# Kernel optimization log

Hardware: AMD Instinct MI355X
Metric: run time of the kernel (lower is better)

The kernel has to match this reference:

```python
import jax, jax.numpy as jnp
import numpy as np

B, S, D = 16, 1024, 128
V = 100000
N = 4096


def _l2norm(x, eps=1e-12):
    # matches torch F.normalize(dim=-1): x / max(||x||, eps)
    n = jnp.sqrt(jnp.sum(x * x, axis=-1, keepdims=True))
    return x / jnp.maximum(n, eps)


def setup_inputs() -> dict:
    key = jax.random.key(0)
    k1, k2, k3, k4, k5 = jax.random.split(key, 5)
    query_embeddings = jax.random.normal(k1, (B, S, D), dtype=jnp.float32)
    key_embeddings = jax.random.normal(k2, (V, D), dtype=jnp.float32)
    loc_b = jax.random.randint(k3, (N,), 0, B)
    loc_s = jax.random.randint(k4, (N,), 0, S)
    label_locations = jnp.stack([loc_b, loc_s], axis=1).astype(jnp.int64)
    labels = jax.random.randint(k5, (N,), 0, V).astype(jnp.int64)
    return {
        "query_embeddings": query_embeddings,
        "key_embeddings": key_embeddings,
        "label_locations": label_locations,
        "labels": labels,
    }


def reference(query_embeddings, key_embeddings, label_locations, labels):
    # gather query vectors at label positions -> [N, D]
    q = query_embeddings[label_locations[:, 0], label_locations[:, 1]]
    q = _l2norm(q)
    k = _l2norm(key_embeddings)
    logits = jnp.einsum("nd,vd->nv", q, k)  # [N, V]
    logZ = jax.nn.logsumexp(logits, axis=-1)  # [N]
    true_logit = jnp.take_along_axis(logits, labels[:, None], axis=-1)[:, 0]
    loss = jnp.mean(logZ - true_logit)  # CrossEntropyLoss mean reduction
    return loss
```

## Files before the change

kernel.cpp:

```cpp
#include <hip/hip_runtime.h>
#include <hip/hip_bf16.h>
#include <hip/hip_fp8.h>

#define S_ 1024
#define D_ 128
#define V_ 100000
#define VSTRIPS_ 3136
#define NPHASE_ 32
#define N_ 4096
#define PADROWS_ 352.0f

typedef __attribute__((ext_vector_type(4))) float f32x4;
typedef __attribute__((ext_vector_type(4))) int   i32x4;
typedef __attribute__((ext_vector_type(8))) int   i32x8;

#define LOG2E_ 1.4426950408889634f
#define LN2_   0.6931471805599453f

__device__ __forceinline__ float exp2_fast(float x) {
#if __has_builtin(__builtin_amdgcn_exp2f)
    return __builtin_amdgcn_exp2f(x);
#else
    return exp2f(x);
#endif
}

__device__ __forceinline__ unsigned char to_fp8(float x) {
    __hip_fp8_e4m3 t(x);
    return (unsigned char)t.__x;
}
__device__ __forceinline__ float from_fp8(unsigned char b) {
    __hip_fp8_e4m3 t; t.__x = (__hip_fp8_storage_t)b;
    return (float)t;
}

__global__ void knorm_kernel(const float* __restrict__ K, char* __restrict__ Kn) {
    __shared__ char sm[4096];
    const int strip = blockIdx.x;
    const int tid = threadIdx.x;
    const int lane = tid & 63;
    const int wvv = tid >> 6;
    char* dst = Kn + (size_t)strip * 4096;
    if (strip >= 3125) {
        *(f32x4*)(dst + tid * 16) = (f32x4){0.f, 0.f, 0.f, 0.f};
        return;
    }
    #pragma unroll
    for (int i = 0; i < 8; ++i) {
        int r = wvv * 8 + i;
        float2 v = ((const float2*)(K + ((size_t)strip * 32 + r) * D_))[lane];
        float ss = v.x * v.x + v.y * v.y;
        #pragma unroll
        for (int off = 32; off; off >>= 1) ss += __shfl_xor(ss, off);
        float rn = rsqrtf(ss);
        unsigned short pk = (unsigned short)to_fp8(v.x * rn)
                          | ((unsigned short)to_fp8(v.y * rn) << 8);
        int addr = ((r >> 4) << 11) + (((lane >> 3) & 1) << 10)
                 + (((lane >> 4) * 16 + (r & 15)) << 4) + ((lane & 7) << 1);
        *(unsigned short*)(sm + addr) = pk;
    }
    __syncthreads();
    *(f32x4*)(dst + tid * 16) = *(const f32x4*)(sm + tid * 16);
}

__global__ void qnorm_kernel(const float* __restrict__ Q, const int* __restrict__ loc,
                             char* __restrict__ Qn, float* __restrict__ Ssum) {
    int w = (blockIdx.x * blockDim.x + threadIdx.x) >> 6;
    int lane = threadIdx.x & 63;
    if (w >= N_) return;
    if (lane == 0) Ssum[w] = 0.f;
    int b = loc[2 * w], s = loc[2 * w + 1];
    float2 v = ((const float2*)(Q + ((size_t)b * S_ + (size_t)s) * D_))[lane];
    float ss = v.x * v.x + v.y * v.y;
    #pragma unroll
    for (int off = 32; off; off >>= 1) ss += __shfl_xor(ss, off);
    float rn = rsqrtf(ss) * LOG2E_;
    unsigned short pk = (unsigned short)to_fp8(v.x * rn)
                      | ((unsigned short)to_fp8(v.y * rn) << 8);
    *(unsigned short*)(Qn + (size_t)w * 128 + 2 * lane) = pk;
}

__global__ __launch_bounds__(256, 2) void ce_main(
    const char* __restrict__ Qn,
    const char* __restrict__ Kn,
    float* __restrict__ Ssum)
{
    const int tid  = threadIdx.x;
    const int lane = tid & 63;
    const int wv   = tid >> 6;
    const int r0   = lane & 15;
    const int hi   = lane >> 4;

    const int fid   = blockIdx.y * 32 + blockIdx.x;
    const int xcd   = fid & 7;
    const int idx   = fid >> 3;
    const int phase = xcd * 4 + (idx >> 5);
    const int qb    = idx & 31;

    i32x8 afr[2];
    {
        const char* qsrc = Qn + ((size_t)qb * 128 + wv * 32 + r0) * 128 + (hi << 5);
        #pragma unroll
        for (int m = 0; m < 2; ++m) {
            i32x4 lo = *(const i32x4*)(qsrc + m * 2048);
            i32x4 hh = *(const i32x4*)(qsrc + m * 2048 + 16);
            afr[m] = (i32x8){lo[0], lo[1], lo[2], lo[3], hh[0], hh[1], hh[2], hh[3]};
        }
    }

    const char* kvbase = Kn + (size_t)phase * 4096 + (lane << 4);

#define LOADSET(B0, B1, j) do {                                              \
        const char* p = kvbase + (size_t)(j) * (4096 * NPHASE_);             \
        i32x4 t0 = *(const i32x4*)(p);                                       \
        i32x4 t1 = *(const i32x4*)(p + 1024);                                \
        i32x4 t2 = *(const i32x4*)(p + 2048);                                \
        i32x4 t3 = *(const i32x4*)(p + 3072);                                \
        B0 = (i32x8){t0[0], t0[1], t0[2], t0[3], t1[0], t1[1], t1[2], t1[3]};\
        B1 = (i32x8){t2[0], t2[1], t2[2], t2[3], t3[0], t3[1], t3[2], t3[3]};\
    } while (0)

#define COMPUTE(B0, B1, ACC) do {                                            \
        __builtin_amdgcn_s_setprio(1);                                       \
        ACC[0][0] = __builtin_amdgcn_mfma_scale_f32_16x16x128_f8f6f4(        \
            afr[0], B0, fz, 0, 0, 0, 127, 0, 127);                           \
        ACC[0][1] = __builtin_amdgcn_mfma_scale_f32_16x16x128_f8f6f4(        \
            afr[0], B1, fz, 0, 0, 0, 127, 0, 127);                           \
        ACC[1][0] = __builtin_amdgcn_mfma_scale_f32_16x16x128_f8f6f4(        \
            afr[1], B0, fz, 0, 0, 0, 127, 0, 127);                           \
        ACC[1][1] = __builtin_amdgcn_mfma_scale_f32_16x16x128_f8f6f4(        \
            afr[1], B1, fz, 0, 0, 0, 127, 0, 127);                           \
        __builtin_amdgcn_s_setprio(0);                                       \
    } while (0)

#define EXP2S(ACC) do {                                                      \
        _Pragma("unroll")                                                    \
        for (int m = 0; m < 2; ++m)                                          \
            _Pragma("unroll")                                                \
            for (int q = 0; q < 4; ++q)                                      \
                psum[m][q] += exp2_fast(ACC[m][0][q]) + exp2_fast(ACC[m][1][q]); \
    } while (0)

    float psum[2][4];
    #pragma unroll
    for (int m = 0; m < 2; ++m)
        #pragma unroll
        for (int q = 0; q < 4; ++q) psum[m][q] = 0.f;

    const f32x4 fz = {0.f, 0.f, 0.f, 0.f};
    f32x4 accE[2][2], accO[2][2];
    #pragma unroll
    for (int m = 0; m < 2; ++m)
        #pragma unroll
        for (int nn = 0; nn < 2; ++nn)
            accO[m][nn] = (f32x4){-16384.f, -16384.f, -16384.f, -16384.f};

    i32x8 RA0, RA1, RB0, RB1;
    LOADSET(RA0, RA1, 0);
    #pragma unroll 1
    for (int j = 0; j < 96; j += 2) {
        LOADSET(RB0, RB1, j + 1);
        EXP2S(accO);
        COMPUTE(RA0, RA1, accE);
        LOADSET(RA0, RA1, j + 2);
        EXP2S(accE);
        COMPUTE(RB0, RB1, accO);
    }
    LOADSET(RB0, RB1, 97);
    EXP2S(accO);
    COMPUTE(RA0, RA1, accE);
    EXP2S(accE);
    COMPUTE(RB0, RB1, accO);
    EXP2S(accO);

#undef LOADSET
#undef COMPUTE
#undef EXP2S

    #pragma unroll
    for (int m = 0; m < 2; ++m) {
        #pragma unroll
        for (int q = 0; q < 4; ++q) {
            float v = psum[m][q];
            v += __shfl_xor(v, 1);
            v += __shfl_xor(v, 2);
            v += __shfl_xor(v, 4);
            v += __shfl_xor(v, 8);
            if (r0 == 0) {
                int row = qb * 128 + wv * 32 + m * 16 + hi * 4 + q;
                atomicAdd(&Ssum[row], v);
            }
        }
    }
}

__global__ void term_kernel(const char* __restrict__ Qn,
                            const char* __restrict__ Kn,
                            const int* __restrict__ labels,
                            const float* __restrict__ Ssum,
                            float* __restrict__ T) {
    int w = (blockIdx.x * blockDim.x + threadIdx.x) >> 6;
    int lane = threadIdx.x & 63;
    if (w >= N_) return;
    int lab = labels[w];
    const unsigned char* qp = (const unsigned char*)(Qn + (size_t)w * 128 + 2 * lane);
    const unsigned char* kp = (const unsigned char*)(Kn
                      + ((size_t)(lab >> 5)) * 4096 + (((lab >> 4) & 1) << 11)
                      + (((lane >> 3) & 1) << 10)
                      + (((lane >> 4) * 16 + (lab & 15)) << 4) + ((lane & 7) << 1));
    float d = from_fp8(qp[0]) * from_fp8(kp[0])
            + from_fp8(qp[1]) * from_fp8(kp[1]);
    #pragma unroll
    for (int off = 32; off; off >>= 1) d += __shfl_xor(d, off);
    if (lane == 0) T[w] = logf(Ssum[w] - PADROWS_) - d * LN2_;
}

__global__ void reduce_kernel(const float* __restrict__ T, float* __restrict__ out) {
    __shared__ float sm[4];
    float s = 0.f;
    for (int i = threadIdx.x; i < N_; i += 256) s += T[i];
    #pragma unroll
    for (int off = 32; off; off >>= 1) s += __shfl_xor(s, off);
    if ((threadIdx.x & 63) == 0) sm[threadIdx.x >> 6] = s;
    __syncthreads();
    if (threadIdx.x == 0) out[0] = (sm[0] + sm[1] + sm[2] + sm[3]) * (1.0f / (float)N_);
}

extern "C" void kernel_launch(void* const* d_in, const int* in_sizes, int n_in,
                              void* d_out, int out_size, void* d_ws, size_t ws_size,
                              hipStream_t stream) {
    (void)in_sizes; (void)n_in; (void)out_size; (void)ws_size;
    const float* Q   = (const float*)d_in[0];
    const float* K   = (const float*)d_in[1];
    const int* loc   = (const int*)d_in[2];
    const int* labels= (const int*)d_in[3];
    float* out = (float*)d_out;

    char* ws = (char*)d_ws;
    char* Kn    = ws;
    char* Qn    = ws + 12845056;
    float* Ssum = (float*)(ws + 12845056 + 524288);
    float* T    = Ssum + N_;

    knorm_kernel<<<VSTRIPS_, 256, 0, stream>>>(K, Kn);
    qnorm_kernel<<<N_ / 4, 256, 0, stream>>>(Q, loc, Qn, Ssum);
    ce_main<<<dim3(32, NPHASE_), 256, 0, stream>>>(Qn, Kn, Ssum);
    term_kernel<<<N_ / 4, 256, 0, stream>>>(Qn, Kn, labels, Ssum, T);
    reduce_kernel<<<1, 256, 0, stream>>>(T, out);
}
```

Baseline: 86.50 us.

## Merge K/Q normalization into one prep kernel and use 32-byte contiguous fp8 tiles

```diff
diff --git a/kernel.cpp b/kernel.cpp
--- a/kernel.cpp
+++ b/kernel.cpp
@@ -34,50 +34,50 @@
     return (float)t;
 }
 
-__global__ void knorm_kernel(const float* __restrict__ K, char* __restrict__ Kn) {
+__global__ void prep_kernel(const float* __restrict__ K, const float* __restrict__ Q,
+                            const int* __restrict__ loc,
+                            char* __restrict__ Kn, char* __restrict__ Qn,
+                            float* __restrict__ Ssum) {
     __shared__ char sm[4096];
-    const int strip = blockIdx.x;
+    const int bid = blockIdx.x;
     const int tid = threadIdx.x;
     const int lane = tid & 63;
     const int wvv = tid >> 6;
-    char* dst = Kn + (size_t)strip * 4096;
-    if (strip >= 3125) {
-        *(f32x4*)(dst + tid * 16) = (f32x4){0.f, 0.f, 0.f, 0.f};
-        return;
-    }
-    #pragma unroll
-    for (int i = 0; i < 8; ++i) {
-        int r = wvv * 8 + i;
-        float2 v = ((const float2*)(K + ((size_t)strip * 32 + r) * D_))[lane];
+    if (bid < VSTRIPS_) {
+        char* dst = Kn + (size_t)bid * 4096;
+        if (bid >= 3125) {
+            *(f32x4*)(dst + tid * 16) = (f32x4){0.f, 0.f, 0.f, 0.f};
+            return;
+        }
+        #pragma unroll
+        for (int i = 0; i < 8; ++i) {
+            int r = wvv * 8 + i;
+            float2 v = ((const float2*)(K + ((size_t)bid * 32 + r) * D_))[lane];
+            float ss = v.x * v.x + v.y * v.y;
+            #pragma unroll
+            for (int off = 32; off; off >>= 1) ss += __shfl_xor(ss, off);
+            float rn = rsqrtf(ss);
+            unsigned short pk = (unsigned short)to_fp8(v.x * rn)
+                              | ((unsigned short)to_fp8(v.y * rn) << 8);
+            int addr = ((r >> 4) << 11) + (((lane >> 4) * 16 + (r & 15)) << 5)
+                     + ((lane & 15) << 1);
+            *(unsigned short*)(sm + addr) = pk;
+        }
+        __syncthreads();
+        *(f32x4*)(dst + tid * 16) = *(const f32x4*)(sm + tid * 16);
+    } else {
+        int w = (bid - VSTRIPS_) * 4 + wvv;
+        if (lane == 0) Ssum[w] = 0.f;
+        int b = loc[2 * w], s = loc[2 * w + 1];
+        float2 v = ((const float2*)(Q + ((size_t)b * S_ + (size_t)s) * D_))[lane];
         float ss = v.x * v.x + v.y * v.y;
         #pragma unroll
         for (int off = 32; off; off >>= 1) ss += __shfl_xor(ss, off);
-        float rn = rsqrtf(ss);
+        float rn = rsqrtf(ss) * LOG2E_;
         unsigned short pk = (unsigned short)to_fp8(v.x * rn)
                           | ((unsigned short)to_fp8(v.y * rn) << 8);
-        int addr = ((r >> 4) << 11) + (((lane >> 3) & 1) << 10)
-                 + (((lane >> 4) * 16 + (r & 15)) << 4) + ((lane & 7) << 1);
-        *(unsigned short*)(sm + addr) = pk;
-    }
-    __syncthreads();
-    *(f32x4*)(dst + tid * 16) = *(const f32x4*)(sm + tid * 16);
-}
-
-__global__ void qnorm_kernel(const float* __restrict__ Q, const int* __restrict__ loc,
-                             char* __restrict__ Qn, float* __restrict__ Ssum) {
-    int w = (blockIdx.x * blockDim.x + threadIdx.x) >> 6;
-    int lane = threadIdx.x & 63;
-    if (w >= N_) return;
-    if (lane == 0) Ssum[w] = 0.f;
-    int b = loc[2 * w], s = loc[2 * w + 1];
-    float2 v = ((const float2*)(Q + ((size_t)b * S_ + (size_t)s) * D_))[lane];
-    float ss = v.x * v.x + v.y * v.y;
-    #pragma unroll
-    for (int off = 32; off; off >>= 1) ss += __shfl_xor(ss, off);
-    float rn = rsqrtf(ss) * LOG2E_;
-    unsigned short pk = (unsigned short)to_fp8(v.x * rn)
-                      | ((unsigned short)to_fp8(v.y * rn) << 8);
-    *(unsigned short*)(Qn + (size_t)w * 128 + 2 * lane) = pk;
+        *(unsigned short*)(Qn + (size_t)w * 128 + 2 * lane) = pk;
+    }
 }
 
 __global__ __launch_bounds__(256, 2) void ce_main(
@@ -100,24 +100,16 @@
     i32x8 afr[2];
     {
         const char* qsrc = Qn + ((size_t)qb * 128 + wv * 32 + r0) * 128 + (hi << 5);
-        #pragma unroll
-        for (int m = 0; m < 2; ++m) {
-            i32x4 lo = *(const i32x4*)(qsrc + m * 2048);
-            i32x4 hh = *(const i32x4*)(qsrc + m * 2048 + 16);
-            afr[m] = (i32x8){lo[0], lo[1], lo[2], lo[3], hh[0], hh[1], hh[2], hh[3]};
-        }
-    }
-
-    const char* kvbase = Kn + (size_t)phase * 4096 + (lane << 4);
+        afr[0] = *(const i32x8*)(qsrc);
+        afr[1] = *(const i32x8*)(qsrc + 2048);
+    }
+
+    const char* kvbase = Kn + (size_t)phase * 4096 + (lane << 5);
 
 #define LOADSET(B0, B1, j) do {                                              \
         const char* p = kvbase + (size_t)(j) * (4096 * NPHASE_);             \
-        i32x4 t0 = *(const i32x4*)(p);                                       \
-        i32x4 t1 = *(const i32x4*)(p + 1024);                                \
-        i32x4 t2 = *(const i32x4*)(p + 2048);                                \
-        i32x4 t3 = *(const i32x4*)(p + 3072);                                \
-        B0 = (i32x8){t0[0], t0[1], t0[2], t0[3], t1[0], t1[1], t1[2], t1[3]};\
-        B1 = (i32x8){t2[0], t2[1], t2[2], t2[3], t3[0], t3[1], t3[2], t3[3]};\
+        B0 = *(const i32x8*)(p);                                             \
+        B1 = *(const i32x8*)(p + 2048);                                      \
     } while (0)
 
 #define COMPUTE(B0, B1, ACC) do {                                            \
@@ -206,8 +198,7 @@
     const unsigned char* qp = (const unsigned char*)(Qn + (size_t)w * 128 + 2 * lane);
     const unsigned char* kp = (const unsigned char*)(Kn
                       + ((size_t)(lab >> 5)) * 4096 + (((lab >> 4) & 1) << 11)
-                      + (((lane >> 3) & 1) << 10)
-                      + (((lane >> 4) * 16 + (lab & 15)) << 4) + ((lane & 7) << 1));
+                      + (((lane >> 4) * 16 + (lab & 15)) << 5) + ((lane & 15) << 1));
     float d = from_fp8(qp[0]) * from_fp8(kp[0])
             + from_fp8(qp[1]) * from_fp8(kp[1]);
     #pragma unroll
@@ -242,8 +233,7 @@
     float* Ssum = (float*)(ws + 12845056 + 524288);
     float* T    = Ssum + N_;
 
-    knorm_kernel<<<VSTRIPS_, 256, 0, stream>>>(K, Kn);
-    qnorm_kernel<<<N_ / 4, 256, 0, stream>>>(Q, loc, Qn, Ssum);
+    prep_kernel<<<VSTRIPS_ + N_ / 4, 256, 0, stream>>>(K, Q, loc, Kn, Qn, Ssum);
     ce_main<<<dim3(32, NPHASE_), 256, 0, stream>>>(Qn, Kn, Ssum);
     term_kernel<<<N_ / 4, 256, 0, stream>>>(Qn, Kn, labels, Ssum, T);
     reduce_kernel<<<1, 256, 0, stream>>>(T, out);
```

New measurement: 83.87 us. 3.0% less time.
